# Kernel tuning notes

Measured on AMD Instinct MI355X. Metric: run time of the kernel, lower is better.

The kernel has to match this reference:

```python
import jax, jax.numpy as jnp
import numpy as np

B, D, K, A, P = 4096, 512, 128, 32, 16  # batch, theta dim, mixture comps, alpha dim, hutchinson probes


def setup_inputs() -> dict:
    key = jax.random.key(0)
    k1, k2, k3, k4 = jax.random.split(key, 4)
    thetas = jax.random.normal(k1, (B, D), dtype=jnp.float32)
    alpha = jax.random.normal(k2, (K, A), dtype=jnp.float32)
    W = jax.random.normal(k3, (A, D), dtype=jnp.float32) / jnp.sqrt(jnp.float32(A))
    v_int = jax.random.randint(k4, (P, B, D), 0, 2, dtype=jnp.int32)  # -> Rademacher via 2v-1
    return {"thetas": thetas, "alpha": alpha, "W": W, "v_int": v_int,
            "N_dataset": 100000, "K_alpha_samples": K}


def _log_density(thetas, alpha, W, N_dataset, K_alpha):
    # Tempered Gaussian mixture: mu_k = alpha_k @ W;
    # logp_b = (N/(N+1)) * (logsumexp_k -0.5||theta_b - mu_k||^2 - log K)
    mu = alpha @ W                                        # [K, D]
    # ||t - mu||^2 expanded to avoid a [B,K,D] intermediate
    sq = (jnp.sum(thetas * thetas, -1, keepdims=True)
          - 2.0 * thetas @ mu.T
          + jnp.sum(mu * mu, -1)[None, :])                # [B, K]
    temper = jnp.float32(N_dataset) / (jnp.float32(N_dataset) + 1.0)
    return temper * (jax.nn.logsumexp(-0.5 * sq, axis=1) - jnp.log(jnp.float32(K_alpha)))


def reference(thetas, alpha, W, v_int, N_dataset, K_alpha_samples):
    v = (2 * v_int - 1).astype(thetas.dtype)              # [P, B, D] Rademacher

    def logp_sum(t):
        return jnp.sum(_log_density(t, alpha, W, N_dataset, K_alpha_samples))

    score = jax.grad(logp_sum)                            # gradiente wrt thetas
    g = score(thetas)                                     # [B, D]

    # Hutchinson trace of the per-sample Hessian via forward-over-reverse HVPs,
    # batched over probes (fuses the torch per-probe autograd.grad loop).
    def hvp(vi):
        return jax.jvp(score, (thetas,), (vi,))[1]        # [B, D]

    Hv = jax.vmap(hvp)(v)                                 # [P, B, D]
    traces = jnp.mean(jnp.sum(v * Hv, axis=-1), axis=0)   # [B]

    loss = 0.5 * jnp.sum(g * g, axis=-1) + traces         # [B]
    return jnp.mean(loss)
```

## Files before the change

### kernel.cpp

```cpp
#include <hip/hip_runtime.h>
#include <hip/hip_bf16.h>
#include <stdint.h>

#define Bsz 4096
#define Dn  512
#define Kn  128
#define Pn  16
#define An  32
#define TB  16

typedef __attribute__((ext_vector_type(4))) float  floatx4;
typedef __attribute__((ext_vector_type(8))) short  shortx8;

__device__ __forceinline__ unsigned short f2bf(float x) {
    union { float f; uint32_t u; } v; v.f = x;
    uint32_t u = v.u;
    uint32_t r = (u + 0x7FFFu + ((u >> 16) & 1u)) >> 16;
    return (unsigned short)r;
}

__global__ __launch_bounds__(256) void k_mu(const float* __restrict__ alpha,
                                            const float* __restrict__ W,
                                            unsigned short* __restrict__ mu_bf,
                                            float* __restrict__ munorm,
                                            float* __restrict__ out) {
    __shared__ float al[An];
    __shared__ float red[4];
    int k = blockIdx.x, t = threadIdx.x;
    if (k == 0 && t == 0) *out = 0.f;
    if (t < An) al[t] = alpha[k * An + t];
    __syncthreads();
    int d0 = t, d1 = t + 256;
    float a0 = 0.f, a1 = 0.f;
#pragma unroll
    for (int a = 0; a < An; ++a) {
        float av = al[a];
        a0 = fmaf(av, W[a * Dn + d0], a0);
        a1 = fmaf(av, W[a * Dn + d1], a1);
    }
    mu_bf[k * Dn + d0] = f2bf(a0);  mu_bf[k * Dn + d1] = f2bf(a1);
    float nrm = a0 * a0 + a1 * a1;
#pragma unroll
    for (int msk = 1; msk < 64; msk <<= 1) nrm += __shfl_xor(nrm, msk);
    if ((t & 63) == 0) red[t >> 6] = nrm;
    __syncthreads();
    if (t == 0) munorm[k] = red[0] + red[1] + red[2] + red[3];
}

__global__ __launch_bounds__(512) void k_gram(const unsigned short* __restrict__ mu_bf,
                                              unsigned short* __restrict__ G_bf) {
    __shared__ short at[TB][520];
    const int tid = threadIdx.x;
    const int lane = tid & 63;
    const int wv = tid >> 6;
    const int m = lane & 15;
    const int q = lane >> 4;
    const int i0 = blockIdx.x * TB;

    const int r = tid >> 5, c0 = (tid & 31) * 16;
    const int4* src = (const int4*)(mu_bf + (size_t)(i0 + r) * Dn + c0);
    *(int4*)&at[r][c0]     = src[0];
    *(int4*)&at[r][c0 + 8] = src[1];

    const int kcol = wv * 16 + m;
    shortx8 bfrag[16];
    const unsigned short* mb = mu_bf + (size_t)kcol * Dn + q * 8;
#pragma unroll
    for (int dc = 0; dc < 16; ++dc) bfrag[dc] = *(const shortx8*)(mb + dc * 32);
    __syncthreads();

    floatx4 acc = {0.f, 0.f, 0.f, 0.f};
#pragma unroll
    for (int dc = 0; dc < 16; ++dc) {
        shortx8 a = *(const shortx8*)&at[m][dc * 32 + q * 8];
        acc = __builtin_amdgcn_mfma_f32_16x16x32_bf16(a, bfrag[dc], acc, 0, 0, 0);
    }
#pragma unroll
    for (int i = 0; i < 4; ++i)
        G_bf[(size_t)(i0 + q * 4 + i) * Kn + kcol] = f2bf(acc[i]);
}

__global__ __launch_bounds__(512, 4) void k_main(
    const float* __restrict__ thetas,
    const int* __restrict__ v_int,
    const unsigned short* __restrict__ mu_bf,
    const float* __restrict__ munorm,
    const unsigned short* __restrict__ G_bf,
    const int* __restrict__ Np,
    float* __restrict__ out)
{
    __shared__ short vt[2][TB][520];
    __shared__ float S_l[TB][132];
    __shared__ float w_l[TB][132];
    __shared__ short wbf[TB][136];
    __shared__ float part[2][8][TB][2];
    __shared__ float thn[TB];
    __shared__ float SwS[TB];

    const int tid = threadIdx.x;
    const int lane = tid & 63;
    const int wv = tid >> 6;
    const int m = lane & 15;
    const int q = lane >> 4;

    const int tileb = blockIdx.x >> 1;
    const int phalf = blockIdx.x & 1;
    const int b0 = tileb * TB;
    const int p0 = phalf * 8;

    const float Nf = (float)(*Np);
    const float temper = Nf / (Nf + 1.0f);

    const int kcol = wv * 16 + m;
    shortx8 mufrag[16];
    {
        const unsigned short* mb = mu_bf + (size_t)kcol * Dn + q * 8;
#pragma unroll
        for (int dc = 0; dc < 16; ++dc)
            mufrag[dc] = *(const shortx8*)(mb + dc * 32);
    }

    const int r = tid >> 5;
    const int c0 = (tid & 31) * 16;
    const size_t PB = (size_t)Bsz * Dn;
    const int* vrow = v_int + (size_t)(b0 + r) * Dn + c0;

    int4 buf[4];
    {
        const int4* g = (const int4*)(vrow + (size_t)p0 * PB);
#pragma unroll
        for (int j = 0; j < 4; ++j) buf[j] = g[j];
    }
    {
        const float4* tg = (const float4*)(thetas + (size_t)(b0 + r) * Dn + c0);
        float tn = 0.f;
#pragma unroll
        for (int j = 0; j < 4; ++j) {
            float4 f = tg[j];
            tn += f.x * f.x + f.y * f.y + f.z * f.z + f.w * f.w;
            short4 h;
            h.x = (short)f2bf(f.x); h.y = (short)f2bf(f.y);
            h.z = (short)f2bf(f.z); h.w = (short)f2bf(f.w);
            *(short4*)&vt[0][r][c0 + j * 4] = h;
        }
#pragma unroll
        for (int msk = 1; msk < 32; msk <<= 1) tn += __shfl_xor(tn, msk);
        if ((tid & 31) == 0) thn[r] = tn;
    }
    __syncthreads();

    {
        floatx4 acc = {0.f, 0.f, 0.f, 0.f};
#pragma unroll
        for (int dc = 0; dc < 16; ++dc) {
            shortx8 a = *(const shortx8*)&vt[0][m][dc * 32 + q * 8];
            acc = __builtin_amdgcn_mfma_f32_16x16x32_bf16(a, mufrag[dc], acc, 0, 0, 0);
        }
#pragma unroll
        for (int i = 0; i < 4; ++i) S_l[q * 4 + i][kcol] = acc[i];
    }
    __syncthreads();

    {
        const int b = tid >> 5, s = tid & 31;
        float l[4];
        float mx = -3.4e38f;
        float tnb = thn[b];
#pragma unroll
        for (int j = 0; j < 4; ++j) {
            int k = s + 32 * j;
            l[j] = -0.5f * (tnb - 2.f * S_l[b][k] + munorm[k]);
            mx = fmaxf(mx, l[j]);
        }
#pragma unroll
        for (int msk = 1; msk < 32; msk <<= 1) mx = fmaxf(mx, __shfl_xor(mx, msk));
        float se = 0.f, ses = 0.f;
        float e[4];
#pragma unroll
        for (int j = 0; j < 4; ++j) {
            int k = s + 32 * j;
            e[j] = __expf(l[j] - mx);
            se += e[j];
            ses += e[j] * S_l[b][k];
        }
#pragma unroll
        for (int msk = 1; msk < 32; msk <<= 1) { se += __shfl_xor(se, msk); ses += __shfl_xor(ses, msk); }
        float inv = 1.f / se;
#pragma unroll
        for (int j = 0; j < 4; ++j) {
            int k = s + 32 * j;
            float wvv = e[j] * inv;
            w_l[b][k] = wvv;
            wbf[b][k] = (short)f2bf(wvv);
        }
        if (s == 0) SwS[b] = ses * inv;
    }
    __syncthreads();

    {
        shortx8 gfrag[4];
        const unsigned short* gb = G_bf + (size_t)kcol * Kn + q * 8;
#pragma unroll
        for (int kc = 0; kc < 4; ++kc) gfrag[kc] = *(const shortx8*)(gb + kc * 32);
        floatx4 acc = {0.f, 0.f, 0.f, 0.f};
#pragma unroll
        for (int kc = 0; kc < 4; ++kc) {
            shortx8 a = *(const shortx8*)&wbf[m][kc * 32 + q * 8];
            acc = __builtin_amdgcn_mfma_f32_16x16x32_bf16(a, gfrag[kc], acc, 0, 0, 0);
        }
        float sg[4];
#pragma unroll
        for (int i = 0; i < 4; ++i) sg[i] = w_l[q * 4 + i][kcol] * acc[i];
#pragma unroll
        for (int msk = 1; msk < 16; msk <<= 1) {
#pragma unroll
            for (int i = 0; i < 4; ++i) sg[i] += __shfl_xor(sg[i], msk);
        }
        if (m == 0) {
#pragma unroll
            for (int i = 0; i < 4; ++i) part[0][wv][q * 4 + i][0] = sg[i];
        }
    }
    __syncthreads();

    float lossA = 0.f, tracc = 0.f;
    if (tid < TB) {
        float wGw = 0.f;
#pragma unroll
        for (int w8 = 0; w8 < 8; ++w8) wGw += part[0][w8][tid][0];
        if (phalf == 0)
            lossA = 0.5f * temper * temper * (wGw - 2.f * SwS[tid] + thn[tid])
                    - temper * (float)Dn;
    }

#pragma unroll
    for (int p = 0; p < 8; ++p) {
#pragma unroll
        for (int j = 0; j < 4; ++j) {
            int4 w4 = buf[j];
            short4 h;
            h.x = (short)(0x3F80 | ((w4.x ^ 1) << 15));
            h.y = (short)(0x3F80 | ((w4.y ^ 1) << 15));
            h.z = (short)(0x3F80 | ((w4.z ^ 1) << 15));
            h.w = (short)(0x3F80 | ((w4.w ^ 1) << 15));
            *(short4*)&vt[p & 1][r][c0 + j * 4] = h;
        }
        __syncthreads();
        if (p < 7) {
            const int4* g = (const int4*)(vrow + (size_t)(p0 + p + 1) * PB);
#pragma unroll
            for (int j = 0; j < 4; ++j) buf[j] = g[j];
        }
        if (p > 0 && tid < TB) {
            float S1 = 0.f, S2 = 0.f;
#pragma unroll
            for (int w8 = 0; w8 < 8; ++w8) {
                S1 += part[(p - 1) & 1][w8][tid][0];
                S2 += part[(p - 1) & 1][w8][tid][1];
            }
            tracc += S1 - S2 * S2;
        }
        floatx4 acc = {0.f, 0.f, 0.f, 0.f};
#pragma unroll
        for (int dc = 0; dc < 16; ++dc) {
            shortx8 a = *(const shortx8*)&vt[p & 1][m][dc * 32 + q * 8];
            acc = __builtin_amdgcn_mfma_f32_16x16x32_bf16(a, mufrag[dc], acc, 0, 0, 0);
        }
        float s1[4], s2[4];
#pragma unroll
        for (int i = 0; i < 4; ++i) {
            float T = acc[i];
            float wt = w_l[q * 4 + i][kcol];
            s1[i] = wt * T * T;
            s2[i] = wt * T;
        }
#pragma unroll
        for (int msk = 1; msk < 16; msk <<= 1) {
#pragma unroll
            for (int i = 0; i < 4; ++i) {
                s1[i] += __shfl_xor(s1[i], msk);
                s2[i] += __shfl_xor(s2[i], msk);
            }
        }
        if (m == 0) {
#pragma unroll
            for (int i = 0; i < 4; ++i) {
                part[p & 1][wv][q * 4 + i][0] = s1[i];
                part[p & 1][wv][q * 4 + i][1] = s2[i];
            }
        }
    }
    __syncthreads();
    if (tid < TB) {
        float S1 = 0.f, S2 = 0.f;
#pragma unroll
        for (int w8 = 0; w8 < 8; ++w8) {
            S1 += part[1][w8][tid][0];
            S2 += part[1][w8][tid][1];
        }
        tracc += S1 - S2 * S2;
        float res = temper * tracc * (1.0f / (float)Pn) + lossA;
#pragma unroll
        for (int msk = 1; msk < 16; msk <<= 1) res += __shfl_xor(res, msk);
        if (tid == 0) atomicAdd(out, res * (1.0f / (float)Bsz));
    }
}

extern "C" void kernel_launch(void* const* d_in, const int* in_sizes, int n_in,
                              void* d_out, int out_size, void* d_ws, size_t ws_size,
                              hipStream_t stream) {
    const float* thetas = (const float*)d_in[0];
    const float* alpha  = (const float*)d_in[1];
    const float* W      = (const float*)d_in[2];
    const int*   v_int  = (const int*)d_in[3];
    const int*   Np     = (const int*)d_in[4];

    char* ws = (char*)d_ws;
    unsigned short* mu_bf  = (unsigned short*)ws;
    float*          munorm = (float*)(ws + 131072);
    unsigned short* G_bf   = (unsigned short*)(ws + 131072 + 1024);

    float* out = (float*)d_out;
    k_mu  <<<dim3(Kn), dim3(256), 0, stream>>>(alpha, W, mu_bf, munorm, out);
    k_gram<<<dim3(8),  dim3(512), 0, stream>>>(mu_bf, G_bf);
    k_main<<<dim3(512), dim3(512), 0, stream>>>(thetas, v_int, mu_bf, munorm, G_bf, Np, out);
}
```

Measured before the change: 217.9 us.

## Swap MFMA operand order to reduce along lanes and accumulate S1 in registers

The MFMA operands are swapped so each lane holds results for one batch row across several mixture components. The per-probe reduction over k then needs only two cross-lane shuffles instead of a 4-step butterfly on eight values. The S1 term is summed in registers across all probes and written to shared memory once, and the weights are cached in registers. This removes most shuffle and LDS traffic in the probe loop. S_l moves to a transposed padded layout, and the Rademacher bf16 encoding is simplified to a single shift-xor.

```diff
diff --git a/kernel.cpp b/kernel.cpp
--- a/kernel.cpp
+++ b/kernel.cpp
@@ -90,10 +90,11 @@
     float* __restrict__ out)
 {
     __shared__ short vt[2][TB][520];
-    __shared__ float S_l[TB][132];
+    __shared__ float S_l[Kn][21];
     __shared__ float w_l[TB][132];
     __shared__ short wbf[TB][136];
-    __shared__ float part[2][8][TB][2];
+    __shared__ float ps2[2][8][TB];
+    __shared__ float ps1[8][TB];
     __shared__ float thn[TB];
     __shared__ float SwS[TB];
 
@@ -153,11 +154,11 @@
         floatx4 acc = {0.f, 0.f, 0.f, 0.f};
 #pragma unroll
         for (int dc = 0; dc < 16; ++dc) {
-            shortx8 a = *(const shortx8*)&vt[0][m][dc * 32 + q * 8];
-            acc = __builtin_amdgcn_mfma_f32_16x16x32_bf16(a, mufrag[dc], acc, 0, 0, 0);
-        }
-#pragma unroll
-        for (int i = 0; i < 4; ++i) S_l[q * 4 + i][kcol] = acc[i];
+            shortx8 bfr = *(const shortx8*)&vt[0][m][dc * 32 + q * 8];
+            acc = __builtin_amdgcn_mfma_f32_16x16x32_bf16(mufrag[dc], bfr, acc, 0, 0, 0);
+        }
+#pragma unroll
+        for (int i = 0; i < 4; ++i) S_l[wv * 16 + q * 4 + i][m] = acc[i];
     }
     __syncthreads();
 
@@ -169,7 +170,7 @@
 #pragma unroll
         for (int j = 0; j < 4; ++j) {
             int k = s + 32 * j;
-            l[j] = -0.5f * (tnb - 2.f * S_l[b][k] + munorm[k]);
+            l[j] = -0.5f * (tnb - 2.f * S_l[k][b] + munorm[k]);
             mx = fmaxf(mx, l[j]);
         }
 #pragma unroll
@@ -181,7 +182,7 @@
             int k = s + 32 * j;
             e[j] = __expf(l[j] - mx);
             se += e[j];
-            ses += e[j] * S_l[b][k];
+            ses += e[j] * S_l[k][b];
         }
 #pragma unroll
         for (int msk = 1; msk < 32; msk <<= 1) { se += __shfl_xor(se, msk); ses += __shfl_xor(ses, msk); }
@@ -197,6 +198,10 @@
     }
     __syncthreads();
 
+    float wreg[4];
+#pragma unroll
+    for (int i = 0; i < 4; ++i) wreg[i] = w_l[m][wv * 16 + q * 4 + i];
+
     {
         shortx8 gfrag[4];
         const unsigned short* gb = G_bf + (size_t)kcol * Kn + q * 8;
@@ -205,44 +210,38 @@
         floatx4 acc = {0.f, 0.f, 0.f, 0.f};
 #pragma unroll
         for (int kc = 0; kc < 4; ++kc) {
-            shortx8 a = *(const shortx8*)&wbf[m][kc * 32 + q * 8];
-            acc = __builtin_amdgcn_mfma_f32_16x16x32_bf16(a, gfrag[kc], acc, 0, 0, 0);
-        }
-        float sg[4];
-#pragma unroll
-        for (int i = 0; i < 4; ++i) sg[i] = w_l[q * 4 + i][kcol] * acc[i];
-#pragma unroll
-        for (int msk = 1; msk < 16; msk <<= 1) {
-#pragma unroll
-            for (int i = 0; i < 4; ++i) sg[i] += __shfl_xor(sg[i], msk);
-        }
-        if (m == 0) {
-#pragma unroll
-            for (int i = 0; i < 4; ++i) part[0][wv][q * 4 + i][0] = sg[i];
-        }
-    }
-    __syncthreads();
-
-    float lossA = 0.f, tracc = 0.f;
+            shortx8 bfr = *(const shortx8*)&wbf[m][kc * 32 + q * 8];
+            acc = __builtin_amdgcn_mfma_f32_16x16x32_bf16(gfrag[kc], bfr, acc, 0, 0, 0);
+        }
+        float sg = wreg[0] * acc[0] + wreg[1] * acc[1] + wreg[2] * acc[2] + wreg[3] * acc[3];
+        sg += __shfl_xor(sg, 16);
+        sg += __shfl_xor(sg, 32);
+        if (q == 0) ps2[0][wv][m] = sg;
+    }
+    __syncthreads();
+
+    float lossA = 0.f;
     if (tid < TB) {
         float wGw = 0.f;
 #pragma unroll
-        for (int w8 = 0; w8 < 8; ++w8) wGw += part[0][w8][tid][0];
+        for (int w8 = 0; w8 < 8; ++w8) wGw += ps2[0][w8][tid];
         if (phalf == 0)
             lossA = 0.5f * temper * temper * (wGw - 2.f * SwS[tid] + thn[tid])
                     - temper * (float)Dn;
     }
 
+    float S1s = 0.f;
+    float sqacc = 0.f;
 #pragma unroll
     for (int p = 0; p < 8; ++p) {
 #pragma unroll
         for (int j = 0; j < 4; ++j) {
             int4 w4 = buf[j];
             short4 h;
-            h.x = (short)(0x3F80 | ((w4.x ^ 1) << 15));
-            h.y = (short)(0x3F80 | ((w4.y ^ 1) << 15));
-            h.z = (short)(0x3F80 | ((w4.z ^ 1) << 15));
-            h.w = (short)(0x3F80 | ((w4.w ^ 1) << 15));
+            h.x = (short)((w4.x << 15) ^ 0xBF80);
+            h.y = (short)((w4.y << 15) ^ 0xBF80);
+            h.z = (short)((w4.z << 15) ^ 0xBF80);
+            h.w = (short)((w4.w << 15) ^ 0xBF80);
             *(short4*)&vt[p & 1][r][c0 + j * 4] = h;
         }
         __syncthreads();
@@ -252,54 +251,44 @@
             for (int j = 0; j < 4; ++j) buf[j] = g[j];
         }
         if (p > 0 && tid < TB) {
-            float S1 = 0.f, S2 = 0.f;
-#pragma unroll
-            for (int w8 = 0; w8 < 8; ++w8) {
-                S1 += part[(p - 1) & 1][w8][tid][0];
-                S2 += part[(p - 1) & 1][w8][tid][1];
-            }
-            tracc += S1 - S2 * S2;
+            float s2c = 0.f;
+#pragma unroll
+            for (int w8 = 0; w8 < 8; ++w8) s2c += ps2[(p - 1) & 1][w8][tid];
+            sqacc += s2c * s2c;
         }
         floatx4 acc = {0.f, 0.f, 0.f, 0.f};
 #pragma unroll
         for (int dc = 0; dc < 16; ++dc) {
-            shortx8 a = *(const shortx8*)&vt[p & 1][m][dc * 32 + q * 8];
-            acc = __builtin_amdgcn_mfma_f32_16x16x32_bf16(a, mufrag[dc], acc, 0, 0, 0);
-        }
-        float s1[4], s2[4];
+            shortx8 bfr = *(const shortx8*)&vt[p & 1][m][dc * 32 + q * 8];
+            acc = __builtin_amdgcn_mfma_f32_16x16x32_bf16(mufrag[dc], bfr, acc, 0, 0, 0);
+        }
+        float s2p = 0.f;
 #pragma unroll
         for (int i = 0; i < 4; ++i) {
             float T = acc[i];
-            float wt = w_l[q * 4 + i][kcol];
-            s1[i] = wt * T * T;
-            s2[i] = wt * T;
-        }
-#pragma unroll
-        for (int msk = 1; msk < 16; msk <<= 1) {
-#pragma unroll
-            for (int i = 0; i < 4; ++i) {
-                s1[i] += __shfl_xor(s1[i], msk);
-                s2[i] += __shfl_xor(s2[i], msk);
-            }
-        }
-        if (m == 0) {
-#pragma unroll
-            for (int i = 0; i < 4; ++i) {
-                part[p & 1][wv][q * 4 + i][0] = s1[i];
-                part[p & 1][wv][q * 4 + i][1] = s2[i];
-            }
-        }
-    }
-    __syncthreads();
+            float wT = wreg[i] * T;
+            s2p += wT;
+            S1s = fmaf(wT, T, S1s);
+        }
+        s2p += __shfl_xor(s2p, 16);
+        s2p += __shfl_xor(s2p, 32);
+        if (q == 0) ps2[p & 1][wv][m] = s2p;
+    }
+
+    S1s += __shfl_xor(S1s, 16);
+    S1s += __shfl_xor(S1s, 32);
+    if (q == 0) ps1[wv][m] = S1s;
+    __syncthreads();
+
     if (tid < TB) {
-        float S1 = 0.f, S2 = 0.f;
+        float s2c = 0.f, S1tot = 0.f;
 #pragma unroll
         for (int w8 = 0; w8 < 8; ++w8) {
-            S1 += part[1][w8][tid][0];
-            S2 += part[1][w8][tid][1];
-        }
-        tracc += S1 - S2 * S2;
-        float res = temper * tracc * (1.0f / (float)Pn) + lossA;
+            s2c += ps2[1][w8][tid];
+            S1tot += ps1[w8][tid];
+        }
+        sqacc += s2c * s2c;
+        float res = temper * (S1tot - sqacc) * (1.0f / (float)Pn) + lossA;
 #pragma unroll
         for (int msk = 1; msk < 16; msk <<= 1) res += __shfl_xor(res, msk);
         if (tid == 0) atomicAdd(out, res * (1.0f / (float)Bsz));
```

New measurement: 219.9 us. No clear change (+0.9%).
